# Kernel optimization log

Hardware: AMD Instinct MI355X
Metric: run time of the kernel (lower is better)

The kernel has to match this reference:

```python
import jax, jax.numpy as jnp
import numpy as np

H = 8          # num heads
DK = 64        # d_model // H
D_MODEL = 512
WIN = 256


def setup_inputs() -> dict:
    key = jax.random.key(0)
    ks = jax.random.split(key, 12)
    B, S = 2, 2048
    mk = lambda k, shape, s=1.0: jax.random.normal(k, shape, dtype=jnp.float32) * s
    inp = {
        "query": mk(ks[0], (B, S, D_MODEL)),
        "key_in": mk(ks[1], (B, S, D_MODEL)),
        "value": mk(ks[2], (B, S, D_MODEL)),
        # nn.Linear(d_model, d_model) weights (out,in) and biases, x4
        "Wq": mk(ks[3], (D_MODEL, D_MODEL), 0.02), "bq": jnp.zeros((D_MODEL,), jnp.float32),
        "Wk": mk(ks[4], (D_MODEL, D_MODEL), 0.02), "bk": jnp.zeros((D_MODEL,), jnp.float32),
        "Wv": mk(ks[5], (D_MODEL, D_MODEL), 0.02), "bv": jnp.zeros((D_MODEL,), jnp.float32),
        "Wo": mk(ks[6], (D_MODEL, D_MODEL), 0.02), "bo": jnp.zeros((D_MODEL,), jnp.float32),
    }
    return inp


def reference(query, key_in, value, Wq, bq, Wk, bk, Wv, bv, Wo, bo):
    B, S, D = query.shape
    scale = np.float32(1.0 / np.sqrt(DK))

    def proj(x, W, b):
        # (B,S,D) -> (B,H,S,DK)
        return (x @ W.T + b).reshape(B, S, H, DK).transpose(0, 2, 1, 3)

    q = proj(query, Wq, bq)
    k = proj(key_in, Wk, bk)
    v = proj(value, Wv, bv)

    # Faithful to naive_masked_matmul: full (B,H,S,S) scores, with entries
    # OUTSIDE the sliding window left at exactly 0.0 (NOT -inf) before softmax.
    scores = jnp.einsum('bhid,bhjd->bhij', q, k) * scale
    idx = jnp.arange(S)
    band = jnp.abs(idx[:, None] - idx[None, :]) <= (WIN // 2)  # (S,S) bool
    scores = jnp.where(band, scores, jnp.float32(0.0))

    p_attn = jax.nn.softmax(scores, axis=-1)
    x = jnp.einsum('bhij,bhjd->bhid', p_attn, v)          # (B,H,S,DK)
    x = x.transpose(0, 2, 1, 3).reshape(B, S, D)          # (B,S,D)
    return x @ Wo.T + bo
```

## Files before the change

### kernel.cpp

```cpp
#include <hip/hip_runtime.h>
#include <hip/hip_bf16.h>

#define SS 2048
#define DD 512
#define HWIN 128

typedef __bf16 bf16x8 __attribute__((ext_vector_type(8)));
typedef unsigned short u16x8 __attribute__((ext_vector_type(8)));
typedef float f32x4 __attribute__((ext_vector_type(4)));

__device__ __forceinline__ unsigned short f2bf(float x) {
    unsigned u = __builtin_bit_cast(unsigned, x);
    return (unsigned short)((u + 0x7fffu + ((u >> 16) & 1u)) >> 16);
}
__device__ __forceinline__ float bf2f(unsigned short s) {
    unsigned u = ((unsigned)s) << 16;
    return __builtin_bit_cast(float, u);
}
__device__ __forceinline__ void split_bf(float x, unsigned short& h, unsigned short& l) {
    h = f2bf(x);
    l = f2bf(x - bf2f(h));
}
__device__ __forceinline__ void split8(float4 f0, float4 f1, u16x8& h, u16x8& l) {
    const float vals[8] = {f0.x, f0.y, f0.z, f0.w, f1.x, f1.y, f1.z, f1.w};
    #pragma unroll
    for (int i = 0; i < 8; ++i) {
        unsigned short hh, ll;
        split_bf(vals[i], hh, ll);
        h[i] = hh;
        l[i] = ll;
    }
}
__device__ __forceinline__ f32x4 mfma16(u16x8 a, u16x8 b, f32x4 c) {
    return __builtin_amdgcn_mfma_f32_16x16x32_bf16(
        __builtin_bit_cast(bf16x8, a), __builtin_bit_cast(bf16x8, b), c, 0, 0, 0);
}
__device__ __forceinline__ void gload16(const unsigned short* g, unsigned short* l) {
    __builtin_amdgcn_global_load_lds(
        (const __attribute__((address_space(1))) unsigned int*)g,
        (__attribute__((address_space(3))) unsigned int*)l, 16, 0, 0);
}

__global__ __launch_bounds__(256) void castAll(
    const float* __restrict__ q, const float* __restrict__ k, const float* __restrict__ v,
    const float* __restrict__ wq, const float* __restrict__ wk,
    const float* __restrict__ wv, const float* __restrict__ wo,
    unsigned short* __restrict__ QAh, unsigned short* __restrict__ KAh,
    unsigned short* __restrict__ AVp,
    unsigned short* __restrict__ WQh, unsigned short* __restrict__ WKh,
    unsigned short* __restrict__ WVp, unsigned short* __restrict__ WoP,
    float* __restrict__ VS)
{
    if (blockIdx.x == 0) {
        float4 zz = {0.f, 0.f, 0.f, 0.f};
        *(float4*)(VS + threadIdx.x * 4) = zz;
    }
    const size_t e0 = ((size_t)blockIdx.x * 256 + threadIdx.x) * 8;
    const float* src; size_t off; unsigned short* dsth; bool paired;
    if      (e0 < 2097152) { src = q; off = e0;           dsth = QAh + off;     paired = false; }
    else if (e0 < 4194304) { src = k; off = e0 - 2097152; dsth = KAh + off;     paired = false; }
    else if (e0 < 6291456) { src = v; off = e0 - 4194304; dsth = AVp + 2 * off; paired = true;  }
    else {
        const size_t e = e0 - 6291456;
        if      (e < 262144) { src = wq; off = e;          dsth = WQh + off;                paired = false; }
        else if (e < 524288) { src = wk; off = e - 262144; dsth = WKh + off;                paired = false; }
        else if (e < 786432) { src = wv; off = e - 524288; dsth = WVp + 2 * (e - 524288);   paired = true;  }
        else                 { src = wo; off = e - 786432; dsth = WoP + 2 * (e - 786432);   paired = true;  }
    }
    u16x8 h, l;
    split8(*(const float4*)(src + off), *(const float4*)(src + off + 4), h, l);
    *(u16x8*)dsth = h;
    if (paired) *(u16x8*)(dsth + 8) = l;
}

__global__ __launch_bounds__(256) void proj_gemm(
    const unsigned short* __restrict__ QAh, const unsigned short* __restrict__ KAh,
    const unsigned short* __restrict__ AVp,
    const unsigned short* __restrict__ WQh, const unsigned short* __restrict__ WKh,
    const unsigned short* __restrict__ WVp,
    const float* __restrict__ bq, const float* __restrict__ bk, const float* __restrict__ bv,
    unsigned short* __restrict__ base,
    unsigned short* __restrict__ VTH, float* __restrict__ VS)
{
    const int d = blockIdx.x;
    const int hi = d >> 6, low = d & 63;
    const int x = low >> 3, rsw = low & 7;
    const int g = hi * 8 + rsw;
    const int y = g / 3, z = g - y * 3;

    const float* bias = (z == 0) ? bq : ((z == 1) ? bk : bv);
    unsigned short* OH = base + (size_t)z * 4194304;

    const int m0 = y * 128, n0 = x * 64;

    __shared__ unsigned short Ah[8 * 64 * 8], Al[8 * 64 * 8];
    __shared__ unsigned short Bh[4 * 64 * 8], Bl[4 * 64 * 8];

    const int tid = threadIdx.x, wave = tid >> 6, lane = tid & 63;
    const int lm = lane & 15, lq = lane >> 4;
    const int wm = wave >> 1, wn = wave & 1;
    const int kb = lq * 8;

    f32x4 acc[4][2] = {};

    const int ar0 = m0 + (wave * 2 + 0) * 16 + lm;
    const int ar1 = m0 + (wave * 2 + 1) * 16 + lm;
    const int br  = n0 + wave * 16 + lm;

    const int aoff0 = ((wave * 2 + 0) * 64 + lane) * 8;
    const int aoff1 = ((wave * 2 + 1) * 64 + lane) * 8;
    const int boff  = (wave * 64 + lane) * 8;

    if (z < 2) {
        const unsigned short* Ap = (z == 0) ? QAh : KAh;
        const unsigned short* Wp = (z == 0) ? WQh : WKh;
        for (int k0 = 0; k0 < 512; k0 += 32) {
            __syncthreads();
            gload16(Ap + (size_t)ar0 * 512 + k0 + kb, &Ah[aoff0]);
            gload16(Ap + (size_t)ar1 * 512 + k0 + kb, &Ah[aoff1]);
            gload16(Wp + (size_t)br  * 512 + k0 + kb, &Bh[boff]);
            __syncthreads();

            u16x8 afh[4], bfh[2];
            #pragma unroll
            for (int i = 0; i < 4; ++i)
                afh[i] = *(const u16x8*)&Ah[((wm * 4 + i) * 64 + lane) * 8];
            #pragma unroll
            for (int j = 0; j < 2; ++j)
                bfh[j] = *(const u16x8*)&Bh[((wn * 2 + j) * 64 + lane) * 8];
            #pragma unroll
            for (int i = 0; i < 4; ++i)
                #pragma unroll
                for (int j = 0; j < 2; ++j)
                    acc[i][j] = mfma16(afh[i], bfh[j], acc[i][j]);
        }
        #pragma unroll
        for (int i = 0; i < 4; ++i)
            #pragma unroll
            for (int j = 0; j < 2; ++j) {
                const int col = n0 + (wn * 2 + j) * 16 + lm;
                const float bv_ = bias[col];
                #pragma unroll
                for (int r = 0; r < 4; ++r) {
                    const int row = m0 + (wm * 4 + i) * 16 + lq * 4 + r;
                    OH[(size_t)row * 512 + col] = f2bf(acc[i][j][r] + bv_);
                }
            }
    } else {
        for (int k0 = 0; k0 < 512; k0 += 32) {
            __syncthreads();
            {
                const unsigned short* pa0 = AVp + 2 * ((size_t)ar0 * 512 + k0 + kb);
                gload16(pa0,     &Ah[aoff0]);
                gload16(pa0 + 8, &Al[aoff0]);
                const unsigned short* pa1 = AVp + 2 * ((size_t)ar1 * 512 + k0 + kb);
                gload16(pa1,     &Ah[aoff1]);
                gload16(pa1 + 8, &Al[aoff1]);
                const unsigned short* pw = WVp + 2 * ((size_t)br * 512 + k0 + kb);
                gload16(pw,     &Bh[boff]);
                gload16(pw + 8, &Bl[boff]);
            }
            __syncthreads();

            u16x8 afh[4], afl[4], bfh[2], bfl[2];
            #pragma unroll
            for (int i = 0; i < 4; ++i) {
                afh[i] = *(const u16x8*)&Ah[((wm * 4 + i) * 64 + lane) * 8];
                afl[i] = *(const u16x8*)&Al[((wm * 4 + i) * 64 + lane) * 8];
            }
            #pragma unroll
            for (int j = 0; j < 2; ++j) {
                bfh[j] = *(const u16x8*)&Bh[((wn * 2 + j) * 64 + lane) * 8];
                bfl[j] = *(const u16x8*)&Bl[((wn * 2 + j) * 64 + lane) * 8];
            }
            #pragma unroll
            for (int i = 0; i < 4; ++i)
                #pragma unroll
                for (int j = 0; j < 2; ++j) {
                    acc[i][j] = mfma16(afh[i], bfh[j], acc[i][j]);
                    acc[i][j] = mfma16(afh[i], bfl[j], acc[i][j]);
                    acc[i][j] = mfma16(afl[i], bfh[j], acc[i][j]);
                }
        }

        float csum[2] = {0.f, 0.f};
        #pragma unroll
        for (int i = 0; i < 4; ++i)
            #pragma unroll
            for (int j = 0; j < 2; ++j) {
                const int col = n0 + (wn * 2 + j) * 16 + lm;
                const float bv_ = bias[col];
                #pragma unroll
                for (int r = 0; r < 4; ++r) {
                    const int row = m0 + (wm * 4 + i) * 16 + lq * 4 + r;
                    const float vv = acc[i][j][r] + bv_;
                    csum[j] += vv;
                    const size_t vix =
                        (((size_t)(row >> 11) * 8 + (col >> 6)) * 64 + (col & 63)) * 2048
                        + (row & 2047);
                    VTH[vix] = f2bf(vv);
                }
            }
        #pragma unroll
        for (int j = 0; j < 2; ++j) {
            float s = csum[j];
            s += __shfl_xor(s, 16);
            s += __shfl_xor(s, 32);
            if (lq == 0) {
                const int col = n0 + (wn * 2 + j) * 16 + lm;
                atomicAdd(&VS[(m0 >> 11) * 512 + col], s);
            }
        }
    }
}

__global__ __launch_bounds__(256) void out_gemm(
    const unsigned short* __restrict__ XHg, const unsigned short* __restrict__ XLg,
    const unsigned short* __restrict__ WoP, const float* __restrict__ bo,
    float* __restrict__ O)
{
    const int gid = blockIdx.x;
    const int rr = gid & 7, hi = gid >> 3;
    const int nblk = hi & 7, mhi = hi >> 3;
    const int mblk = mhi * 8 + rr;
    const int m0 = mblk * 64, n0 = nblk * 64;

    __shared__ unsigned short Ah[2 * 4096], Al[2 * 4096];
    __shared__ unsigned short Bh[2 * 4096], Bl[2 * 4096];

    const int tid = threadIdx.x, wave = tid >> 6, lane = tid & 63;
    const int lm = lane & 15, lq = lane >> 4;
    const int kb = lq * 8;

    f32x4 acc[4] = {};

    const int arow = m0 + wave * 16 + lm;
    const int brow = n0 + wave * 16 + lm;

    #define OSTAGE(k0_, bs)                                                     \
    {                                                                           \
        _Pragma("unroll")                                                       \
        for (int s = 0; s < 2; ++s) {                                           \
            const int o = (bs) * 4096 + ((s * 4 + wave) * 64 + lane) * 8;       \
            gload16(XHg + (size_t)arow * 512 + (k0_) + s * 32 + kb, &Ah[o]);    \
            gload16(XLg + (size_t)arow * 512 + (k0_) + s * 32 + kb, &Al[o]);    \
            const unsigned short* pw =                                          \
                WoP + 2 * ((size_t)brow * 512 + (k0_) + s * 32 + kb);           \
            gload16(pw,     &Bh[o]);                                            \
            gload16(pw + 8, &Bl[o]);                                            \
        }                                                                       \
    }

    OSTAGE(0, 0);
    __syncthreads();

    for (int t = 0; t < 8; ++t) {
        const int cur = t & 1;
        if (t < 7) OSTAGE((t + 1) * 64, cur ^ 1);

        #pragma unroll
        for (int s = 0; s < 2; ++s) {
            const u16x8 a_h = *(const u16x8*)&Ah[cur * 4096 + ((s * 4 + wave) * 64 + lane) * 8];
            const u16x8 a_l = *(const u16x8*)&Al[cur * 4096 + ((s * 4 + wave) * 64 + lane) * 8];
            #pragma unroll
            for (int j = 0; j < 4; ++j) {
                const u16x8 b_h = *(const u16x8*)&Bh[cur * 4096 + ((s * 4 + j) * 64 + lane) * 8];
                const u16x8 b_l = *(const u16x8*)&Bl[cur * 4096 + ((s * 4 + j) * 64 + lane) * 8];
                acc[j] = mfma16(a_h, b_h, acc[j]);
                acc[j] = mfma16(a_h, b_l, acc[j]);
                acc[j] = mfma16(a_l, b_h, acc[j]);
            }
        }

        __syncthreads();
    }
    #undef OSTAGE

    #pragma unroll
    for (int j = 0; j < 4; ++j) {
        const int col = n0 + j * 16 + lm;
        const float bv_ = bo[col];
        #pragma unroll
        for (int r = 0; r < 4; ++r) {
            const int row = m0 + wave * 16 + lq * 4 + r;
            O[(size_t)row * 512 + col] = acc[j][r] + bv_;
        }
    }
}

__global__ __launch_bounds__(256) void attn_mfma(
    const unsigned short* __restrict__ QH, const unsigned short* __restrict__ KH,
    const unsigned short* __restrict__ VTH, const float* __restrict__ VS,
    unsigned short* __restrict__ XH, unsigned short* __restrict__ XL)
{
    const int dblk = blockIdx.x;
    const int bhi = dblk >> 8, blow = dblk & 255;
    const int xblk = blow >> 3, rrs = blow & 7;
    const int bh = bhi * 8 + rrs;
    const int h = bh & 7, b = bh >> 3;
    const int i0 = xblk * 64;
    const int tid = threadIdx.x, wave = tid >> 6, lane = tid & 63;
    const int lm = lane & 15, lq = lane >> 4;
    const int kb = lq * 8;

    __shared__ unsigned short KfH[2 * 8 * 64 * 8];
    __shared__ unsigned short VfH[2 * 8 * 64 * 8];
    __shared__ unsigned short Swh[64][72];

    const size_t qoff = ((size_t)(b * SS + i0 + wave * 16 + lm)) * DD + h * 64 + kb;
    const u16x8 aQ0h = *(const u16x8*)(QH + qoff);
    const u16x8 aQ1h = *(const u16x8*)(QH + qoff + 32);

    f32x4 oacc[4] = {};
    float dacc[4] = {0.f, 0.f, 0.f, 0.f};

    const size_t vrow = ((size_t)bh * 64 + wave * 16 + lm) * 2048;
    const int s0 = (wave * 2 + 0) * 64 * 8 + lane * 8;
    const int s1 = (wave * 2 + 1) * 64 * 8 + lane * 8;

    #define STAGE(jt_, bufsel)                                                  \
    {                                                                           \
        const int jt0_ = i0 - 128 + (jt_) * 64;                                 \
        const int jrow = jt0_ + wave * 16 + lm;                                 \
        const int jrc = min(max(jrow, 0), SS - 1);                              \
        const size_t kgb = ((size_t)(b * SS + jrc)) * DD + h * 64 + kb;         \
        gload16(KH + kgb,      &KfH[(bufsel) * 4096 + s0]);                     \
        gload16(KH + kgb + 32, &KfH[(bufsel) * 4096 + s1]);                     \
        const int j0c = min(max(jt0_ + kb, 0), SS - 8);                         \
        const int j1c = min(max(jt0_ + 32 + kb, 0), SS - 8);                    \
        gload16(VTH + vrow + j0c, &VfH[(bufsel) * 4096 + s0]);                  \
        gload16(VTH + vrow + j1c, &VfH[(bufsel) * 4096 + s1]);                  \
    }

    STAGE(0, 0);
    __syncthreads();

    for (int jt = 0; jt < 5; ++jt) {
        const int buf = jt & 1;
        if (jt < 4) STAGE(jt + 1, buf ^ 1);
        const int jt0 = i0 - 128 + jt * 64;

        #pragma unroll
        for (int js = 0; js < 4; ++js) {
            const int j0 = js * 16;
            const u16x8 bK0h = *(const u16x8*)&KfH[buf * 4096 + ((js * 2 + 0) * 64 + lane) * 8];
            const u16x8 bK1h = *(const u16x8*)&KfH[buf * 4096 + ((js * 2 + 1) * 64 + lane) * 8];
            f32x4 s = {0.f, 0.f, 0.f, 0.f};
            s = mfma16(aQ0h, bK0h, s);
            s = mfma16(aQ1h, bK1h, s);
            const int jg = jt0 + j0 + lm;
            const int iq = i0 + wave * 16 + lq * 4;
            #pragma unroll
            for (int r = 0; r < 4; ++r) {
                const int qi = iq + r;
                const bool in = (jg >= 0) && (jg < SS) &&
                                (jg >= qi - HWIN) && (jg <= qi + HWIN);
                const float w = in ? (__expf(s[r] * 0.125f) - 1.0f) : 0.0f;
                dacc[r] += w;
                Swh[wave * 16 + lq * 4 + r][j0 + lm] = f2bf(w);
            }
        }

        const u16x8 aP0h = *(const u16x8*)&Swh[wave * 16 + lm][kb];
        const u16x8 aP1h = *(const u16x8*)&Swh[wave * 16 + lm][kb + 32];
        #pragma unroll
        for (int s4 = 0; s4 < 4; ++s4) {
            const u16x8 bV0h = *(const u16x8*)&VfH[buf * 4096 + ((s4 * 2 + 0) * 64 + lane) * 8];
            const u16x8 bV1h = *(const u16x8*)&VfH[buf * 4096 + ((s4 * 2 + 1) * 64 + lane) * 8];
            oacc[s4] = mfma16(aP0h, bV0h, oacc[s4]);
            oacc[s4] = mfma16(aP1h, bV1h, oacc[s4]);
        }
        __syncthreads();
    }
    #undef STAGE

    #pragma unroll
    for (int r = 0; r < 4; ++r) {
        float v = dacc[r];
        v += __shfl_xor(v, 1);
        v += __shfl_xor(v, 2);
        v += __shfl_xor(v, 4);
        v += __shfl_xor(v, 8);
        dacc[r] = v + 2048.0f;
    }

    #pragma unroll
    for (int s4 = 0; s4 < 4; ++s4) {
        const float vsv = VS[bh * 64 + s4 * 16 + lm];
        #pragma unroll
        for (int r = 0; r < 4; ++r) {
            const int qrow = i0 + wave * 16 + lq * 4 + r;
            const float x = (oacc[s4][r] + vsv) / dacc[r];
            unsigned short xh, xl;
            split_bf(x, xh, xl);
            const size_t ix = ((size_t)(b * SS + qrow)) * DD + h * 64 + s4 * 16 + lm;
            XH[ix] = xh;
            XL[ix] = xl;
        }
    }
}

extern "C" void kernel_launch(void* const* d_in, const int* in_sizes, int n_in,
                              void* d_out, int out_size, void* d_ws, size_t ws_size,
                              hipStream_t stream)
{
    const float* query  = (const float*)d_in[0];
    const float* key_in = (const float*)d_in[1];
    const float* value  = (const float*)d_in[2];
    const float* Wq = (const float*)d_in[3]; const float* bq = (const float*)d_in[4];
    const float* Wk = (const float*)d_in[5]; const float* bk = (const float*)d_in[6];
    const float* Wv = (const float*)d_in[7]; const float* bv = (const float*)d_in[8];
    const float* Wo = (const float*)d_in[9]; const float* bo = (const float*)d_in[10];

    unsigned short* wsb = (unsigned short*)d_ws;
    unsigned short* QH  = wsb;
    unsigned short* KH  = wsb + 4194304;
    unsigned short* VTH = wsb + 8388608;
    unsigned short* XH  = wsb + 12582912;
    unsigned short* XL  = wsb + 14680064;
    unsigned short* WQh = wsb + 16777216;
    unsigned short* WKh = wsb + 17039360;
    unsigned short* WVp = wsb + 17301504;
    unsigned short* WoP = wsb + 17825792;
    unsigned short* QAh = wsb + 18350080;
    unsigned short* KAh = wsb + 20447232;
    unsigned short* AVp = wsb + 22544384;
    float* VSp  = (float*)((char*)d_ws + 63045632);

    castAll<<<3584, 256, 0, stream>>>(query, key_in, value, Wq, Wk, Wv, Wo,
                                      QAh, KAh, AVp, WQh, WKh, WVp, WoP, VSp);

    proj_gemm<<<768, 256, 0, stream>>>(QAh, KAh, AVp, WQh, WKh, WVp,
                                       bq, bk, bv, QH, VTH, VSp);

    attn_mfma<<<512, 256, 0, stream>>>(QH, KH, VTH, VSp, XH, XL);

    out_gemm<<<512, 256, 0, stream>>>(XH, XL, WoP, bo, (float*)d_out);
}
```

Baseline: 151.4 us.

## Drop split-bf16 precision for V projection and skip fully masked score tiles

The value input and Wv are now cast to a single bf16 array instead of hi/lo pairs, so the V projection runs the same one-MFMA-per-step loop as Q and K rather than three MFMAs with double loads. Separately, the attention kernel skips QK^T MFMAs and exp for 16x16 score subtiles that lie entirely outside the band or the sequence bounds, writing zeros instead. The first change cuts memory traffic and matrix work in the cast and projection stages, at the cost of V precision. The second removes wasted compute in edge tiles.

```diff
diff --git a/kernel.cpp b/kernel.cpp
--- a/kernel.cpp
+++ b/kernel.cpp
@@ -20,16 +20,6 @@
 __device__ __forceinline__ void split_bf(float x, unsigned short& h, unsigned short& l) {
     h = f2bf(x);
     l = f2bf(x - bf2f(h));
-}
-__device__ __forceinline__ void split8(float4 f0, float4 f1, u16x8& h, u16x8& l) {
-    const float vals[8] = {f0.x, f0.y, f0.z, f0.w, f1.x, f1.y, f1.z, f1.w};
-    #pragma unroll
-    for (int i = 0; i < 8; ++i) {
-        unsigned short hh, ll;
-        split_bf(vals[i], hh, ll);
-        h[i] = hh;
-        l[i] = ll;
-    }
 }
 __device__ __forceinline__ f32x4 mfma16(u16x8 a, u16x8 b, f32x4 c) {
     return __builtin_amdgcn_mfma_f32_16x16x32_bf16(
@@ -46,9 +36,9 @@
     const float* __restrict__ wq, const float* __restrict__ wk,
     const float* __restrict__ wv, const float* __restrict__ wo,
     unsigned short* __restrict__ QAh, unsigned short* __restrict__ KAh,
-    unsigned short* __restrict__ AVp,
+    unsigned short* __restrict__ VAh,
     unsigned short* __restrict__ WQh, unsigned short* __restrict__ WKh,
-    unsigned short* __restrict__ WVp, unsigned short* __restrict__ WoP,
+    unsigned short* __restrict__ WVh, unsigned short* __restrict__ WoP,
     float* __restrict__ VS)
 {
     if (blockIdx.x == 0) {
@@ -56,28 +46,36 @@
         *(float4*)(VS + threadIdx.x * 4) = zz;
     }
     const size_t e0 = ((size_t)blockIdx.x * 256 + threadIdx.x) * 8;
-    const float* src; size_t off; unsigned short* dsth; bool paired;
-    if      (e0 < 2097152) { src = q; off = e0;           dsth = QAh + off;     paired = false; }
-    else if (e0 < 4194304) { src = k; off = e0 - 2097152; dsth = KAh + off;     paired = false; }
-    else if (e0 < 6291456) { src = v; off = e0 - 4194304; dsth = AVp + 2 * off; paired = true;  }
+    const float* src; size_t off; unsigned short* dsth; bool paired = false;
+    if      (e0 < 2097152) { src = q; off = e0;           dsth = QAh + off; }
+    else if (e0 < 4194304) { src = k; off = e0 - 2097152; dsth = KAh + off; }
+    else if (e0 < 6291456) { src = v; off = e0 - 4194304; dsth = VAh + off; }
     else {
         const size_t e = e0 - 6291456;
-        if      (e < 262144) { src = wq; off = e;          dsth = WQh + off;                paired = false; }
-        else if (e < 524288) { src = wk; off = e - 262144; dsth = WKh + off;                paired = false; }
-        else if (e < 786432) { src = wv; off = e - 524288; dsth = WVp + 2 * (e - 524288);   paired = true;  }
-        else                 { src = wo; off = e - 786432; dsth = WoP + 2 * (e - 786432);   paired = true;  }
-    }
-    u16x8 h, l;
-    split8(*(const float4*)(src + off), *(const float4*)(src + off + 4), h, l);
+        if      (e < 262144) { src = wq; off = e;          dsth = WQh + off; }
+        else if (e < 524288) { src = wk; off = e - 262144; dsth = WKh + off; }
+        else if (e < 786432) { src = wv; off = e - 524288; dsth = WVh + off; }
+        else { src = wo; off = e - 786432; dsth = WoP + 2 * (e - 786432); paired = true; }
+    }
+    const float4 f0 = *(const float4*)(src + off), f1 = *(const float4*)(src + off + 4);
+    const float vals[8] = {f0.x, f0.y, f0.z, f0.w, f1.x, f1.y, f1.z, f1.w};
+    u16x8 h;
+    #pragma unroll
+    for (int i = 0; i < 8; ++i) h[i] = f2bf(vals[i]);
     *(u16x8*)dsth = h;
-    if (paired) *(u16x8*)(dsth + 8) = l;
+    if (paired) {
+        u16x8 l;
+        #pragma unroll
+        for (int i = 0; i < 8; ++i) l[i] = f2bf(vals[i] - bf2f(h[i]));
+        *(u16x8*)(dsth + 8) = l;
+    }
 }
 
 __global__ __launch_bounds__(256) void proj_gemm(
     const unsigned short* __restrict__ QAh, const unsigned short* __restrict__ KAh,
-    const unsigned short* __restrict__ AVp,
+    const unsigned short* __restrict__ VAh,
     const unsigned short* __restrict__ WQh, const unsigned short* __restrict__ WKh,
-    const unsigned short* __restrict__ WVp,
+    const unsigned short* __restrict__ WVh,
     const float* __restrict__ bq, const float* __restrict__ bk, const float* __restrict__ bv,
     unsigned short* __restrict__ base,
     unsigned short* __restrict__ VTH, float* __restrict__ VS)
@@ -88,13 +86,15 @@
     const int g = hi * 8 + rsw;
     const int y = g / 3, z = g - y * 3;
 
+    const unsigned short* Ap = (z == 0) ? QAh : ((z == 1) ? KAh : VAh);
+    const unsigned short* Wp = (z == 0) ? WQh : ((z == 1) ? WKh : WVh);
     const float* bias = (z == 0) ? bq : ((z == 1) ? bk : bv);
     unsigned short* OH = base + (size_t)z * 4194304;
 
     const int m0 = y * 128, n0 = x * 64;
 
-    __shared__ unsigned short Ah[8 * 64 * 8], Al[8 * 64 * 8];
-    __shared__ unsigned short Bh[4 * 64 * 8], Bl[4 * 64 * 8];
+    __shared__ unsigned short Ah[8 * 64 * 8];
+    __shared__ unsigned short Bh[4 * 64 * 8];
 
     const int tid = threadIdx.x, wave = tid >> 6, lane = tid & 63;
     const int lm = lane & 15, lq = lane >> 4;
@@ -111,29 +111,28 @@
     const int aoff1 = ((wave * 2 + 1) * 64 + lane) * 8;
     const int boff  = (wave * 64 + lane) * 8;
 
-    if (z < 2) {
-        const unsigned short* Ap = (z == 0) ? QAh : KAh;
-        const unsigned short* Wp = (z == 0) ? WQh : WKh;
-        for (int k0 = 0; k0 < 512; k0 += 32) {
-            __syncthreads();
-            gload16(Ap + (size_t)ar0 * 512 + k0 + kb, &Ah[aoff0]);
-            gload16(Ap + (size_t)ar1 * 512 + k0 + kb, &Ah[aoff1]);
-            gload16(Wp + (size_t)br  * 512 + k0 + kb, &Bh[boff]);
-            __syncthreads();
-
-            u16x8 afh[4], bfh[2];
-            #pragma unroll
-            for (int i = 0; i < 4; ++i)
-                afh[i] = *(const u16x8*)&Ah[((wm * 4 + i) * 64 + lane) * 8];
+    for (int k0 = 0; k0 < 512; k0 += 32) {
+        __syncthreads();
+        gload16(Ap + (size_t)ar0 * 512 + k0 + kb, &Ah[aoff0]);
+        gload16(Ap + (size_t)ar1 * 512 + k0 + kb, &Ah[aoff1]);
+        gload16(Wp + (size_t)br  * 512 + k0 + kb, &Bh[boff]);
+        __syncthreads();
+
+        u16x8 afh[4], bfh[2];
+        #pragma unroll
+        for (int i = 0; i < 4; ++i)
+            afh[i] = *(const u16x8*)&Ah[((wm * 4 + i) * 64 + lane) * 8];
+        #pragma unroll
+        for (int j = 0; j < 2; ++j)
+            bfh[j] = *(const u16x8*)&Bh[((wn * 2 + j) * 64 + lane) * 8];
+        #pragma unroll
+        for (int i = 0; i < 4; ++i)
             #pragma unroll
             for (int j = 0; j < 2; ++j)
-                bfh[j] = *(const u16x8*)&Bh[((wn * 2 + j) * 64 + lane) * 8];
-            #pragma unroll
-            for (int i = 0; i < 4; ++i)
-                #pragma unroll
-                for (int j = 0; j < 2; ++j)
-                    acc[i][j] = mfma16(afh[i], bfh[j], acc[i][j]);
-        }
+                acc[i][j] = mfma16(afh[i], bfh[j], acc[i][j]);
+    }
+
+    if (z < 2) {
         #pragma unroll
         for (int i = 0; i < 4; ++i)
             #pragma unroll
@@ -147,42 +146,6 @@
                 }
             }
     } else {
-        for (int k0 = 0; k0 < 512; k0 += 32) {
-            __syncthreads();
-            {
-                const unsigned short* pa0 = AVp + 2 * ((size_t)ar0 * 512 + k0 + kb);
-                gload16(pa0,     &Ah[aoff0]);
-                gload16(pa0 + 8, &Al[aoff0]);
-                const unsigned short* pa1 = AVp + 2 * ((size_t)ar1 * 512 + k0 + kb);
-                gload16(pa1,     &Ah[aoff1]);
-                gload16(pa1 + 8, &Al[aoff1]);
-                const unsigned short* pw = WVp + 2 * ((size_t)br * 512 + k0 + kb);
-                gload16(pw,     &Bh[boff]);
-                gload16(pw + 8, &Bl[boff]);
-            }
-            __syncthreads();
-
-            u16x8 afh[4], afl[4], bfh[2], bfl[2];
-            #pragma unroll
-            for (int i = 0; i < 4; ++i) {
-                afh[i] = *(const u16x8*)&Ah[((wm * 4 + i) * 64 + lane) * 8];
-                afl[i] = *(const u16x8*)&Al[((wm * 4 + i) * 64 + lane) * 8];
-            }
-            #pragma unroll
-            for (int j = 0; j < 2; ++j) {
-                bfh[j] = *(const u16x8*)&Bh[((wn * 2 + j) * 64 + lane) * 8];
-                bfl[j] = *(const u16x8*)&Bl[((wn * 2 + j) * 64 + lane) * 8];
-            }
-            #pragma unroll
-            for (int i = 0; i < 4; ++i)
-                #pragma unroll
-                for (int j = 0; j < 2; ++j) {
-                    acc[i][j] = mfma16(afh[i], bfh[j], acc[i][j]);
-                    acc[i][j] = mfma16(afh[i], bfl[j], acc[i][j]);
-                    acc[i][j] = mfma16(afl[i], bfh[j], acc[i][j]);
-                }
-        }
-
         float csum[2] = {0.f, 0.f};
         #pragma unroll
         for (int i = 0; i < 4; ++i)
@@ -339,10 +302,20 @@
         const int buf = jt & 1;
         if (jt < 4) STAGE(jt + 1, buf ^ 1);
         const int jt0 = i0 - 128 + jt * 64;
+        const int rmin = i0 + wave * 16;
 
         #pragma unroll
         for (int js = 0; js < 4; ++js) {
             const int j0 = js * 16;
+            const int cmin = jt0 + j0, cmax = cmin + 15;
+            const bool skip = (cmax < 0) || (cmin >= SS) ||
+                              (cmax < rmin - HWIN) || (cmin > rmin + 15 + HWIN);
+            if (skip) {
+                #pragma unroll
+                for (int r = 0; r < 4; ++r)
+                    Swh[wave * 16 + lq * 4 + r][j0 + lm] = 0;
+                continue;
+            }
             const u16x8 bK0h = *(const u16x8*)&KfH[buf * 4096 + ((js * 2 + 0) * 64 + lane) * 8];
             const u16x8 bK1h = *(const u16x8*)&KfH[buf * 4096 + ((js * 2 + 1) * 64 + lane) * 8];
             f32x4 s = {0.f, 0.f, 0.f, 0.f};
@@ -420,17 +393,17 @@
     unsigned short* XL  = wsb + 14680064;
     unsigned short* WQh = wsb + 16777216;
     unsigned short* WKh = wsb + 17039360;
-    unsigned short* WVp = wsb + 17301504;
+    unsigned short* WVh = wsb + 17301504;
     unsigned short* WoP = wsb + 17825792;
     unsigned short* QAh = wsb + 18350080;
     unsigned short* KAh = wsb + 20447232;
-    unsigned short* AVp = wsb + 22544384;
+    unsigned short* VAh = wsb + 22544384;
     float* VSp  = (float*)((char*)d_ws + 63045632);
 
     castAll<<<3584, 256, 0, stream>>>(query, key_in, value, Wq, Wk, Wv, Wo,
-                                      QAh, KAh, AVp, WQh, WKh, WVp, WoP, VSp);
-
-    proj_gemm<<<768, 256, 0, stream>>>(QAh, KAh, AVp, WQh, WKh, WVp,
+                                      QAh, KAh, VAh, WQh, WKh, WVh, WoP, VSp);
+
+    proj_gemm<<<768, 256, 0, stream>>>(QAh, KAh, VAh, WQh, WKh, WVh,
                                        bq, bk, bv, QH, VTH, VSp);
 
     attn_mfma<<<512, 256, 0, stream>>>(QH, KH, VTH, VSp, XH, XL);
```

Measured after the change: 146.4 us. 3.4% less time.
